# Performance work log

Hardware: AMD Instinct MI355X
Metric: run time of the kernel (lower is better)

Reference implementation:

```python
import jax, jax.numpy as jnp
import numpy as np
from jax import lax

OC = 128      # out_channels
KS = 7        # kernel_size
STRIDE = 2
IMG = 224     # image_size
NS = 7        # num_scales
PAD = KS // 2 # 3
MAXS = 2      # max_scale
EPS = 1e-5
OUT = IMG // STRIDE  # 112
B = 32
DN = ('NCHW', 'OIHW', 'NCHW')


def _windows():
    # Mirrors the torch __init__ window construction (float32 linspace like torch).
    scales = np.linspace(2.0, 1.0, NS, dtype=np.float32)
    borders = np.linspace(0, IMG // 2, NS + 1).astype(np.int64)
    iw = np.empty((NS, 4, 4), dtype=np.int64)
    for s in range(NS):
        a, b = borders[s], borders[s + 1]
        c, d = IMG - b, IMG - a
        iw[s] = np.array([[a, a, b, c], [b, a, d, b], [c, b, d, d], [a, c, c, d]])
    ow = iw // STRIDE  # output windows
    iwp = iw + PAD * MAXS
    iwp = np.stack([(iwp[s].astype(np.float32) / scales[s]).astype(np.int64) for s in range(NS)])
    iwp[:, :, :2] -= PAD
    iwp[:, :, 2:] += PAD
    return iwp, ow

IWP, OW = _windows()


def _bn(x, g, b):
    # BatchNorm2d in training mode: biased batch stats over (N, H, W)
    m = jnp.mean(x, axis=(0, 2, 3), keepdims=True)
    v = jnp.var(x, axis=(0, 2, 3), keepdims=True)
    return g[None, :, None, None] * (x - m) * lax.rsqrt(v + EPS) + b[None, :, None, None]


def _forward(inp, conv_w, gamma1, beta1, conv2_w, gamma2, beta2):
    n = inp.shape[0]
    x = jnp.pad(inp, ((0, 0), (0, 0), (PAD, PAD), (PAD, PAD)))  # ConstantPad2d(3, 0)
    out = jnp.zeros((n, OC, OUT, OUT), inp.dtype)
    for s in range(NS):
        for w in range(4):
            ti, li, bi, ri = (int(v) for v in IWP[s, w])
            crop = x[:, :, ti:bi, li:ri]
            # torch interpolate(bilinear, antialias) to the crop's own size is the identity,
            # since input_window_sizes == (bi-ti, ri-li) exactly.
            f = lax.conv_general_dilated(crop, conv_w, (STRIDE, STRIDE), 'VALID',
                                         dimension_numbers=DN)
            to, lo, bo, ro = (int(v) for v in OW[s, w])
            oh, owid = bo - to, ro - lo
            fh, fw = f.shape[2], f.shape[3]
            # torch 'nearest' (size-based): src = floor(i * in / out)
            ih = (np.arange(oh) * fh) // oh
            iwd = (np.arange(owid) * fw) // owid
            up = f[:, :, ih][:, :, :, iwd]
            out = out.at[:, :, to:bo, lo:ro].set(up)
    h = jax.nn.relu(_bn(out, gamma1, beta1))
    # MaxPool2d(kernel=3, stride=2, padding=1) -> pads with -inf
    h = lax.reduce_window(h, jnp.asarray(-jnp.inf, h.dtype), lax.max,
                          (1, 1, 3, 3), (1, 1, 2, 2),
                          ((0, 0), (0, 0), (1, 1), (1, 1)))
    h = lax.conv_general_dilated(h, conv2_w, (1, 1), ((1, 1), (1, 1)),
                                 dimension_numbers=DN)
    return jax.nn.relu(_bn(h, gamma2, beta2))


def setup_inputs() -> dict:
    key = jax.random.key(0)
    k0, k1, k2 = jax.random.split(key, 3)
    inp = jax.random.normal(k0, (B, 3, IMG, IMG), jnp.float32)
    conv_w = jax.random.normal(k1, (OC, 3, KS, KS), jnp.float32) * 0.05
    conv2_w = jax.random.normal(k2, (OC, OC, 3, 3), jnp.float32) * 0.03
    return {
        'inp': inp,
        'conv_w': conv_w,
        'gamma1': jnp.ones((OC,), jnp.float32),
        'beta1': jnp.zeros((OC,), jnp.float32),
        'conv2_w': conv2_w,
        'gamma2': jnp.ones((OC,), jnp.float32),
        'beta2': jnp.zeros((OC,), jnp.float32),
    }


def reference(inp, conv_w, gamma1, beta1, conv2_w, gamma2, beta2):
    return _forward(inp, conv_w, gamma1, beta1, conv2_w, gamma2, beta2)
```

## Files before the change

### kernel.cpp

```cpp
#include <hip/hip_runtime.h>
#include <hip/hip_bf16.h>
#include <cstdint>

#define IMGSZ 224
#define OUTSZ 112
#define POOLSZ 56
#define OCN 128
#define BN_ 32
#define PIX1 (OUTSZ*OUTSZ)
#define PIX2 (POOLSZ*POOLSZ)
#define HP 58
#define HSTRIDE (HP*HP*OCN)
#define PW 240
#define PH 233
#define PPL (PH*PW)
#define K1C 192

typedef float f32x4 __attribute__((ext_vector_type(4)));
typedef short bf16x8 __attribute__((ext_vector_type(8)));
struct alignas(4) u4a { unsigned x, y, z, w; };

__device__ inline short f2bf(float v) {
    __hip_bfloat16 h = __float2bfloat16(v);
    return *(short*)&h;
}
__device__ inline unsigned pack2bf(float a, float b) {
    return (unsigned short)f2bf(a) | ((unsigned)(unsigned short)f2bf(b) << 16);
}
__device__ inline float bf2f(short s) {
    return __uint_as_float(((unsigned)(unsigned short)s) << 16);
}
__device__ inline bf16x8 ldb8(const short* p) {
    u4a t = *(const u4a*)p;
    union { u4a u; bf16x8 v; } c; c.u = t; return c.v;
}
__device__ inline void gload16(const short* g, short* l) {
    __builtin_amdgcn_global_load_lds((const __attribute__((address_space(1))) void*)g,
                                     (__attribute__((address_space(3))) void*)l, 16, 0, 0);
}

__global__ __launch_bounds__(256) void k_setup(const float* __restrict__ w1,
                                               short* __restrict__ w1b,
                                               const float* __restrict__ w2,
                                               short* __restrict__ w2b,
                                               int2* __restrict__ map,
                                               float* __restrict__ stats,
                                               unsigned* __restrict__ h2p) {
    int blk = blockIdx.x;
    int tid = threadIdx.x;
    if (blk < 49) {
        int p = blk * 256 + tid;
        int oy = p / OUTSZ, ox = p % OUTSZ;
        int e = min(min(oy, ox), min(111 - oy, 111 - ox));
        int s = e >> 3;
        int a = 16 * s, b = a + 16, c = 224 - b, d = 224 - a;
        int ao = a >> 1, bo = b >> 1, co = c >> 1, dd = d >> 1;
        int ti, li, bi, ri;
        if      (oy >= ao && oy < bo && ox >= ao && ox < co) { ti=a; li=a; bi=b; ri=c; }
        else if (oy >= bo && oy < dd && ox >= ao && ox < bo) { ti=b; li=a; bi=d; ri=b; }
        else if (oy >= co && oy < dd && ox >= bo && ox < dd) { ti=c; li=b; bi=d; ri=d; }
        else                                                 { ti=a; li=c; bi=c; ri=d; }
        float scale = (float)(2.0 - (double)s * 0.16666666666666666);
        int tip = (int)((float)(ti + 6) / scale) - 3;
        int lip = (int)((float)(li + 6) / scale) - 3;
        int bip = (int)((float)(bi + 6) / scale) + 3;
        int rip = (int)((float)(ri + 6) / scale) + 3;
        int fh = (bip - tip - 7) / 2 + 1;
        int fw = (rip - lip - 7) / 2 + 1;
        int to = ti >> 1, lo = li >> 1, bo2 = bi >> 1, ro = ri >> 1;
        int i = oy - to, j = ox - lo;
        int pp = (i * fh) / (bo2 - to);
        int qq = (j * fw) / (ro - lo);
        map[p] = make_int2(tip + 2 * pp, lip + 2 * qq);
    } else if (blk < 145) {
        int idx = (blk - 49) * 256 + tid;
        int oc = idx / K1C, k = idx % K1C;
        int g8 = k >> 3, e2 = k & 7;
        float v = 0.f;
        if (g8 < 21 && e2 < 7) {
            int ic = g8 / 7, ky = g8 - ic * 7;
            v = w1[((oc * 3 + ic) * 7 + ky) * 7 + e2];
        }
        w1b[idx] = f2bf(v);
    } else if (blk < 721) {
        int idx = (blk - 145) * 256 + tid;
        int oc = idx / 1152;
        int rem = idx - oc * 1152;
        int ic = rem / 9;
        int s  = rem - ic * 9;
        int t  = s * 2 + (ic >> 6);
        int ic6 = ic & 63;
        int slot = (ic6 >> 3) ^ (oc & 7);
        w2b[t * 8192 + oc * 64 + slot * 8 + (ic6 & 7)] = f2bf(w2[idx]);
    } else if (blk < 785) {
        stats[(blk - 721) * 256 + tid] = 0.f;
    } else {
        int idx = blk - 785;
        int bx = idx % 57, n = idx / 57;
        int c2 = tid & 63, po = tid >> 6;
        int pp = bx * 4 + po;
        int y, x;
        if      (pp < 58)  { y = 0;  x = pp; }
        else if (pp < 116) { y = 57; x = pp - 58; }
        else if (pp < 172) { y = pp - 116 + 1; x = 0; }
        else               { y = pp - 172 + 1; x = 57; }
        h2p[(size_t)n * (HSTRIDE / 2) + (y * HP + x) * 64 + c2] = 0u;
    }
}

__global__ __launch_bounds__(256) void k_pad(const float* __restrict__ inp,
                                             short* __restrict__ padA,
                                             short* __restrict__ padB) {
    int x = threadIdx.x;
    if (x >= PW) return;
    int y = blockIdx.x;
    int pl = blockIdx.y;
    int iy = y - 3;
    bool yok = (unsigned)iy < 224u;
    const float* src = inp + (size_t)pl * 50176 + iy * 224;
    float vA = (yok && (unsigned)(x - 3) < 224u) ? src[x - 3] : 0.f;
    float vB = (yok && (unsigned)(x - 2) < 224u) ? src[x - 2] : 0.f;
    size_t o = (size_t)pl * PPL + y * PW + x;
    padA[o] = f2bf(vA);
    padB[o] = f2bf(vB);
}

__global__ __launch_bounds__(256, 4) void k_conv1m(const short* __restrict__ padA,
                                                   const short* __restrict__ padB,
                                                   const short* __restrict__ w1b,
                                                   const int2* __restrict__ map,
                                                   short* __restrict__ out1b,
                                                   float* __restrict__ sum1x,
                                                   float* __restrict__ sq1x) {
    __shared__ short As[64 * 256];
    __shared__ float sred[4][64][2];
    int tid = threadIdx.x;
    int wave = tid >> 6, lane = tid & 63;
    int q = lane >> 4, l16 = lane & 15;
    int ochalf = blockIdx.x & 1;
    int pxblk = blockIdx.x >> 1;
    int n = blockIdx.y;
    int px0 = pxblk * 128 + wave * 32 + l16;
    int px1 = px0 + 16;
    int2 m0 = map[px0];
    int2 m1 = map[px1];
    size_t bn = (size_t)n * 3 * PPL;
    const short* r0 = ((m0.y & 1) ? padB + (m0.y - 1) : padA + m0.y) + bn + m0.x * PW;
    const short* r1 = ((m1.y & 1) ? padB + (m1.y - 1) : padA + m1.y) + bn + m1.x * PW;

    const short* wsl = w1b + ochalf * 64 * K1C;
#pragma unroll
    for (int i = 0; i < 6; i++) {
        int chunk = tid + i * 256;
        int r = chunk / 24, c = chunk - r * 24;
        u4a v = *(const u4a*)(wsl + r * K1C + c * 8);
        *(u4a*)(As + r * 256 + ((c ^ (r & 15)) * 8)) = v;
    }

    bf16x8 ld[12];
#pragma unroll
    for (int icc = 0; icc < 6; icc++) {
        int g8 = (icc == 5) ? 20 : (icc * 4 + q);
        int ic = (g8 >= 7) + (g8 >= 14);
        int ky = g8 - ic * 7;
        int off = ic * PPL + ky * PW;
        ld[icc * 2]     = ldb8(r0 + off);
        ld[icc * 2 + 1] = ldb8(r1 + off);
    }

    f32x4 acc[4][2];
#pragma unroll
    for (int t = 0; t < 4; t++) { acc[t][0] = (f32x4){0,0,0,0}; acc[t][1] = (f32x4){0,0,0,0}; }

    __syncthreads();

    const short* Abase = As + l16 * 256;
#pragma unroll
    for (int icc = 0; icc < 6; icc++) {
        bf16x8 bf0 = ld[icc * 2];
        bf16x8 bf1 = ld[icc * 2 + 1];
        int pos = ((icc * 4 + q) ^ l16) * 8;
#pragma unroll
        for (int t = 0; t < 4; t++) {
            bf16x8 af = *(const bf16x8*)(Abase + t * 16 * 256 + pos);
            acc[t][0] = __builtin_amdgcn_mfma_f32_16x16x32_bf16(af, bf0, acc[t][0], 0, 0, 0);
            acc[t][1] = __builtin_amdgcn_mfma_f32_16x16x32_bf16(af, bf1, acc[t][1], 0, 0, 0);
        }
    }

    short* ob = out1b + ((size_t)(n * PIX1) + px0) * OCN + ochalf * 64 + q * 4;
#pragma unroll
    for (int t = 0; t < 4; t++) {
#pragma unroll
        for (int g = 0; g < 2; g++) {
            f32x4 a = acc[t][g];
            uint2 u;
            u.x = pack2bf(a[0], a[1]);
            u.y = pack2bf(a[2], a[3]);
            *(uint2*)(ob + (size_t)g * 16 * OCN + t * 16) = u;
        }
    }

#pragma unroll
    for (int t = 0; t < 4; t++) {
#pragma unroll
        for (int r = 0; r < 4; r++) {
            float a0 = acc[t][0][r], a1 = acc[t][1][r];
            float s = a0 + a1;
            float z = fmaf(a0, a0, a1 * a1);
#pragma unroll
            for (int msk = 1; msk < 16; msk <<= 1) {
                s += __shfl_xor(s, msk, 64);
                z += __shfl_xor(z, msk, 64);
            }
            if (l16 == 0) {
                int ocl = t * 16 + q * 4 + r;
                sred[wave][ocl][0] = s;
                sred[wave][ocl][1] = z;
            }
        }
    }
    __syncthreads();
    if (tid < 64) {
        float s = sred[0][tid][0] + sred[1][tid][0] + sred[2][tid][0] + sred[3][tid][0];
        float z = sred[0][tid][1] + sred[1][tid][1] + sred[2][tid][1] + sred[3][tid][1];
        int oc = ochalf * 64 + tid;
        atomicAdd(&sum1x[n * OCN + oc], s);
        atomicAdd(&sq1x[n * OCN + oc], z);
    }
}

__global__ void k_fin2(const float* __restrict__ sumx, const float* __restrict__ sqx,
                       const float* __restrict__ gamma, const float* __restrict__ beta,
                       float invN, float* __restrict__ scale, float* __restrict__ shift) {
    int c = threadIdx.x;
    if (c >= OCN) return;
    float s = 0.f, q = 0.f;
    for (int n = 0; n < BN_; n++) { s += sumx[n * OCN + c]; q += sqx[n * OCN + c]; }
    float m = s * invN;
    float v = q * invN - m * m;
    float sc = gamma[c] * rsqrtf(v + 1e-5f);
    scale[c] = sc;
    shift[c] = beta[c] - m * sc;
}

__global__ __launch_bounds__(256) void k_bnpool(const unsigned* __restrict__ out1b,
                                                const float* __restrict__ scale,
                                                const float* __restrict__ shift,
                                                unsigned* __restrict__ h2p) {
    int tid = threadIdx.x;
    int c2 = tid & 63, po = tid >> 6;
    int pp = blockIdx.x * 4 + po;
    int n = blockIdx.y;
    int py = pp / POOLSZ, px = pp % POOLSZ;
    const unsigned* base = out1b + (size_t)n * PIX1 * 64;
    float sc0 = scale[2 * c2],     sh0 = shift[2 * c2];
    float sc1 = scale[2 * c2 + 1], sh1 = shift[2 * c2 + 1];
    float m0 = -1e30f, m1 = -1e30f;
#pragma unroll
    for (int dy = 0; dy < 3; dy++) {
        int y = 2 * py - 1 + dy;
        if ((unsigned)y >= (unsigned)OUTSZ) continue;
#pragma unroll
        for (int dx = 0; dx < 3; dx++) {
            int x = 2 * px - 1 + dx;
            if ((unsigned)x >= (unsigned)OUTSZ) continue;
            unsigned u = base[(size_t)(y * OUTSZ + x) * 64 + c2];
            float v0 = __uint_as_float(u << 16);
            float v1 = __uint_as_float(u & 0xffff0000u);
            m0 = fmaxf(m0, fmaf(sc0, v0, sh0));
            m1 = fmaxf(m1, fmaf(sc1, v1, sh1));
        }
    }
    m0 = fmaxf(m0, 0.f); m1 = fmaxf(m1, 0.f);
    h2p[(size_t)n * (HSTRIDE / 2) + ((py + 1) * HP + (px + 1)) * 64 + c2] = pack2bf(m0, m1);
}

__global__ __launch_bounds__(256, 4) void k_conv2g(const short* __restrict__ h2p,
                                                   const short* __restrict__ w2b,
                                                   short* __restrict__ out2b,
                                                   float* __restrict__ sum2x,
                                                   float* __restrict__ sq2x) {
    __shared__ short LDSb[15360];
    int tid = threadIdx.x;
    int wave = tid >> 6, lane = tid & 63;
    int q = lane >> 4, l16 = lane & 15;
    int id = blockIdx.x;
    int xcd = id & 7, seq = id >> 3;
    int n = xcd + 8 * (seq / 28);
    int rb = seq % 28;
    int y0 = rb * 2;
    const short* hb = h2p + (size_t)n * HSTRIDE;

    int bofs[4];
#pragma unroll
    for (int i = 0; i < 4; i++) {
        int ck = tid + i * 256;
        if (ck > 895) ck = 895;
        int px = ck >> 3, sl = ck & 7;
        int r = px >= 56;
        int xc = px - (r ? 56 : 0);
        bofs[i] = ((y0 + r) * 58 + xc) * 128 + ((sl ^ (px & 7)) * 8);
    }

    f32x4 acc[2][7];
#pragma unroll
    for (int t16 = 0; t16 < 2; t16++)
#pragma unroll
        for (int g = 0; g < 7; g++) acc[t16][g] = (f32x4){0, 0, 0, 0};

    const short* Az = LDSb;
    const short* Bz = LDSb + 8192;
    int arow0 = (wave * 32 + l16) * 64;
    int arow1 = arow0 + 16 * 64;

    for (int t = 0; t < 18; t++) {
        __syncthreads();
        const short* wt = w2b + t * 8192;
#pragma unroll
        for (int i = 0; i < 4; i++)
            gload16(wt + (tid + i * 256) * 8, &LDSb[(tid + i * 256) * 8]);
        int s = t >> 1, ich = t & 1;
        int dy = s / 3, dx = s - dy * 3;
        int doff = (dy * 58 + dx) * 128 + ich * 64;
#pragma unroll
        for (int i = 0; i < 3; i++)
            gload16(hb + bofs[i] + doff, &LDSb[8192 + (tid + i * 256) * 8]);
        if (tid < 128)
            gload16(hb + bofs[3] + doff, &LDSb[8192 + (tid + 768) * 8]);
        asm volatile("s_waitcnt vmcnt(0)" ::: "memory");
        __syncthreads();
#pragma unroll
        for (int icc2 = 0; icc2 < 2; icc2++) {
            int so = ((icc2 * 4 + q) ^ (l16 & 7)) * 8;
            bf16x8 af0 = *(const bf16x8*)(Az + arow0 + so);
            bf16x8 af1 = *(const bf16x8*)(Az + arow1 + so);
            bf16x8 bf[7];
#pragma unroll
            for (int g = 0; g < 7; g++)
                bf[g] = *(const bf16x8*)(Bz + (g * 16 + l16) * 64 + so);
#pragma unroll
            for (int g = 0; g < 7; g++) {
                acc[0][g] = __builtin_amdgcn_mfma_f32_16x16x32_bf16(af0, bf[g], acc[0][g], 0, 0, 0);
                acc[1][g] = __builtin_amdgcn_mfma_f32_16x16x32_bf16(af1, bf[g], acc[1][g], 0, 0, 0);
            }
        }
    }

    short* ob = out2b + ((size_t)n * PIX2 + y0 * 56) * OCN + wave * 32 + q * 4;
#pragma unroll
    for (int t16 = 0; t16 < 2; t16++) {
#pragma unroll
        for (int g = 0; g < 7; g++) {
            f32x4 a = acc[t16][g];
            uint2 u;
            u.x = pack2bf(a[0], a[1]);
            u.y = pack2bf(a[2], a[3]);
            *(uint2*)(ob + (size_t)(g * 16 + l16) * OCN + t16 * 16) = u;
        }
    }

#pragma unroll
    for (int t16 = 0; t16 < 2; t16++) {
#pragma unroll
        for (int r = 0; r < 4; r++) {
            float sv = 0.f, zv = 0.f;
#pragma unroll
            for (int g = 0; g < 7; g++) {
                float v = acc[t16][g][r];
                sv += v;
                zv = fmaf(v, v, zv);
            }
#pragma unroll
            for (int msk = 1; msk < 16; msk <<= 1) {
                sv += __shfl_xor(sv, msk, 64);
                zv += __shfl_xor(zv, msk, 64);
            }
            if (l16 == 0) {
                int oc = wave * 32 + t16 * 16 + q * 4 + r;
                atomicAdd(&sum2x[n * OCN + oc], sv);
                atomicAdd(&sq2x[n * OCN + oc], zv);
            }
        }
    }
}

__global__ __launch_bounds__(256) void k_bnrelu(const short* __restrict__ in2,
                                                float* __restrict__ y,
                                                const float* __restrict__ scale,
                                                const float* __restrict__ shift) {
    int tid = threadIdx.x;
    int w = tid >> 6, l = tid & 63;
    int pxg = blockIdx.x * 256 + w * 64 + (l & 15) * 4;
    int n = pxg / PIX2;
    int px = pxg - n * PIX2;
    const short* src = in2 + (size_t)pxg * OCN + (l >> 4) * 8;
    float* dst = y + (size_t)n * (OCN * PIX2) + px;
#pragma unroll
    for (int jc = 0; jc < 4; jc++) {
        int c0 = (l >> 4) * 8 + jc * 32;
        bf16x8 v0 = ldb8(src + jc * 32);
        bf16x8 v1 = ldb8(src + OCN + jc * 32);
        bf16x8 v2 = ldb8(src + 2 * OCN + jc * 32);
        bf16x8 v3 = ldb8(src + 3 * OCN + jc * 32);
#pragma unroll
        for (int j = 0; j < 8; j++) {
            float sc = scale[c0 + j], sh = shift[c0 + j];
            float4 o;
            o.x = fmaxf(fmaf(sc, bf2f(v0[j]), sh), 0.f);
            o.y = fmaxf(fmaf(sc, bf2f(v1[j]), sh), 0.f);
            o.z = fmaxf(fmaf(sc, bf2f(v2[j]), sh), 0.f);
            o.w = fmaxf(fmaf(sc, bf2f(v3[j]), sh), 0.f);
            *(float4*)(dst + (size_t)(c0 + j) * PIX2) = o;
        }
    }
}

extern "C" void kernel_launch(void* const* d_in, const int* in_sizes, int n_in,
                              void* d_out, int out_size, void* d_ws, size_t ws_size,
                              hipStream_t stream) {
    const float* inp = (const float*)d_in[0];
    const float* w1  = (const float*)d_in[1];
    const float* g1  = (const float*)d_in[2];
    const float* b1  = (const float*)d_in[3];
    const float* w2  = (const float*)d_in[4];
    const float* g2  = (const float*)d_in[5];
    const float* b2  = (const float*)d_in[6];
    float* out = (float*)d_out;

    char* ws = (char*)d_ws;
    int2*  map   = (int2*)ws;
    float* stats = (float*)(ws + 102400);
    short* w2b   = (short*)(ws + 176128);
    short* w1b   = (short*)(ws + 471040);
    short* padA  = (short*)(ws + 520192);
    short* padB  = (short*)(ws + 11256832ULL);
    short* h2p   = (short*)(ws + 21993472ULL);
    short* out1b = (short*)(ws + 49551360ULL);
    short* out2b = (short*)(ws + 152311808ULL);

    float* sum1x = stats;
    float* sq1x  = stats + 4096;
    float* sum2x = stats + 8192;
    float* sq2x  = stats + 12288;
    float* SC1 = stats + 16384, *SH1 = stats + 16512;
    float* SC2 = stats + 16640, *SH2 = stats + 16768;

    k_setup <<<dim3(2609), 256, 0, stream>>>(w1, w1b, w2, w2b, map, stats, (unsigned*)h2p);
    k_pad   <<<dim3(PH, 96), 256, 0, stream>>>(inp, padA, padB);
    k_conv1m<<<dim3(196, BN_), 256, 0, stream>>>(padA, padB, w1b, map, out1b, sum1x, sq1x);
    k_fin2  <<<1, 128, 0, stream>>>(sum1x, sq1x, g1, b1, 1.f / (BN_ * PIX1), SC1, SH1);
    k_bnpool<<<dim3(PIX2 / 4, BN_), 256, 0, stream>>>((const unsigned*)out1b, SC1, SH1, (unsigned*)h2p);
    k_conv2g<<<dim3(896), 256, 0, stream>>>(h2p, w2b, out2b, sum2x, sq2x);
    k_fin2  <<<1, 128, 0, stream>>>(sum2x, sq2x, g2, b2, 1.f / (BN_ * PIX2), SC2, SH2);
    k_bnrelu<<<dim3(392), 256, 0, stream>>>(out2b, out, SC2, SH2);
}
```

Baseline: 257.5 us.

## Shrink conv tiles and LDS, use DPP row reductions, raise occupancy

Conv1 weight staging switches from a 256-stride XOR swizzle to a compact 192-stride rotated layout, cutting LDS use, and its weight load now issues after the activation loads. Conv2 retiles from two image rows (112 pixels) to 64-pixel linear blocks, with fewer accumulators, a smaller LDS buffer and 1568 blocks instead of 896. Both kernels raise the launch-bounds occupancy hint from 4 to 6 and replace shuffle-xor reductions with DPP row sums. The aim is more resident waves and cheaper reductions to hide latency, at the cost of less weight reuse per block in conv2 and more atomics.

```diff
diff --git a/kernel.cpp b/kernel.cpp
--- a/kernel.cpp
+++ b/kernel.cpp
@@ -37,6 +37,18 @@
 __device__ inline void gload16(const short* g, short* l) {
     __builtin_amdgcn_global_load_lds((const __attribute__((address_space(1))) void*)g,
                                      (__attribute__((address_space(3))) void*)l, 16, 0, 0);
+}
+
+template<int CTRL>
+__device__ inline float dppf(float v) {
+    return __int_as_float(__builtin_amdgcn_update_dpp(0, __float_as_int(v), CTRL, 0xF, 0xF, true));
+}
+__device__ inline float rowsum16(float v) {
+    v += dppf<0xB1>(v);
+    v += dppf<0x4E>(v);
+    v += dppf<0x141>(v);
+    v += dppf<0x140>(v);
+    return v;
 }
 
 __global__ __launch_bounds__(256) void k_setup(const float* __restrict__ w1,
@@ -125,15 +137,15 @@
     padB[o] = f2bf(vB);
 }
 
-__global__ __launch_bounds__(256, 4) void k_conv1m(const short* __restrict__ padA,
+__global__ __launch_bounds__(256, 6) void k_conv1m(const short* __restrict__ padA,
                                                    const short* __restrict__ padB,
                                                    const short* __restrict__ w1b,
                                                    const int2* __restrict__ map,
                                                    short* __restrict__ out1b,
                                                    float* __restrict__ sum1x,
                                                    float* __restrict__ sq1x) {
-    __shared__ short As[64 * 256];
-    __shared__ float sred[4][64][2];
+    __shared__ short As[64 * 192];
+    __shared__ float2 sred[4][64];
     int tid = threadIdx.x;
     int wave = tid >> 6, lane = tid & 63;
     int q = lane >> 4, l16 = lane & 15;
@@ -148,15 +160,6 @@
     const short* r0 = ((m0.y & 1) ? padB + (m0.y - 1) : padA + m0.y) + bn + m0.x * PW;
     const short* r1 = ((m1.y & 1) ? padB + (m1.y - 1) : padA + m1.y) + bn + m1.x * PW;
 
-    const short* wsl = w1b + ochalf * 64 * K1C;
-#pragma unroll
-    for (int i = 0; i < 6; i++) {
-        int chunk = tid + i * 256;
-        int r = chunk / 24, c = chunk - r * 24;
-        u4a v = *(const u4a*)(wsl + r * K1C + c * 8);
-        *(u4a*)(As + r * 256 + ((c ^ (r & 15)) * 8)) = v;
-    }
-
     bf16x8 ld[12];
 #pragma unroll
     for (int icc = 0; icc < 6; icc++) {
@@ -168,21 +171,40 @@
         ld[icc * 2 + 1] = ldb8(r1 + off);
     }
 
+    const short* wsl = w1b + ochalf * 64 * K1C;
+#pragma unroll
+    for (int i = 0; i < 6; i++) {
+        int chunk = tid + i * 256;
+        int r = chunk / 24, c = chunk - r * 24;
+        int rm = r % 24;
+        int sl = c + rm; if (sl >= 24) sl -= 24;
+        u4a v = *(const u4a*)(wsl + r * K1C + c * 8);
+        *(u4a*)(As + r * 192 + sl * 8) = v;
+    }
+
     f32x4 acc[4][2];
 #pragma unroll
     for (int t = 0; t < 4; t++) { acc[t][0] = (f32x4){0,0,0,0}; acc[t][1] = (f32x4){0,0,0,0}; }
 
+    int rowb[4], rowm[4];
+#pragma unroll
+    for (int t = 0; t < 4; t++) {
+        int row = t * 16 + l16;
+        rowb[t] = row * 192;
+        rowm[t] = row % 24;
+    }
+
     __syncthreads();
 
-    const short* Abase = As + l16 * 256;
 #pragma unroll
     for (int icc = 0; icc < 6; icc++) {
         bf16x8 bf0 = ld[icc * 2];
         bf16x8 bf1 = ld[icc * 2 + 1];
-        int pos = ((icc * 4 + q) ^ l16) * 8;
+        int c = icc * 4 + q;
 #pragma unroll
         for (int t = 0; t < 4; t++) {
-            bf16x8 af = *(const bf16x8*)(Abase + t * 16 * 256 + pos);
+            int sl = rowm[t] + c; if (sl >= 24) sl -= 24;
+            bf16x8 af = *(const bf16x8*)(As + rowb[t] + sl * 8);
             acc[t][0] = __builtin_amdgcn_mfma_f32_16x16x32_bf16(af, bf0, acc[t][0], 0, 0, 0);
             acc[t][1] = __builtin_amdgcn_mfma_f32_16x16x32_bf16(af, bf1, acc[t][1], 0, 0, 0);
         }
@@ -206,24 +228,17 @@
 #pragma unroll
         for (int r = 0; r < 4; r++) {
             float a0 = acc[t][0][r], a1 = acc[t][1][r];
-            float s = a0 + a1;
-            float z = fmaf(a0, a0, a1 * a1);
-#pragma unroll
-            for (int msk = 1; msk < 16; msk <<= 1) {
-                s += __shfl_xor(s, msk, 64);
-                z += __shfl_xor(z, msk, 64);
-            }
-            if (l16 == 0) {
-                int ocl = t * 16 + q * 4 + r;
-                sred[wave][ocl][0] = s;
-                sred[wave][ocl][1] = z;
-            }
+            float s = rowsum16(a0 + a1);
+            float z = rowsum16(fmaf(a0, a0, a1 * a1));
+            if (l16 == 0)
+                sred[wave][t * 16 + q * 4 + r] = make_float2(s, z);
         }
     }
     __syncthreads();
     if (tid < 64) {
-        float s = sred[0][tid][0] + sred[1][tid][0] + sred[2][tid][0] + sred[3][tid][0];
-        float z = sred[0][tid][1] + sred[1][tid][1] + sred[2][tid][1] + sred[3][tid][1];
+        float2 p0 = sred[0][tid], p1 = sred[1][tid], p2 = sred[2][tid], p3 = sred[3][tid];
+        float s = p0.x + p1.x + p2.x + p3.x;
+        float z = p0.y + p1.y + p2.y + p3.y;
         int oc = ochalf * 64 + tid;
         atomicAdd(&sum1x[n * OCN + oc], s);
         atomicAdd(&sq1x[n * OCN + oc], z);
@@ -276,38 +291,36 @@
     h2p[(size_t)n * (HSTRIDE / 2) + ((py + 1) * HP + (px + 1)) * 64 + c2] = pack2bf(m0, m1);
 }
 
-__global__ __launch_bounds__(256, 4) void k_conv2g(const short* __restrict__ h2p,
+__global__ __launch_bounds__(256, 6) void k_conv2g(const short* __restrict__ h2p,
                                                    const short* __restrict__ w2b,
                                                    short* __restrict__ out2b,
                                                    float* __restrict__ sum2x,
                                                    float* __restrict__ sq2x) {
-    __shared__ short LDSb[15360];
+    __shared__ short LDSb[12288];
     int tid = threadIdx.x;
     int wave = tid >> 6, lane = tid & 63;
     int q = lane >> 4, l16 = lane & 15;
     int id = blockIdx.x;
     int xcd = id & 7, seq = id >> 3;
-    int n = xcd + 8 * (seq / 28);
-    int rb = seq % 28;
-    int y0 = rb * 2;
+    int n = xcd + 8 * (seq / 49);
+    int px0 = (seq % 49) * 64;
     const short* hb = h2p + (size_t)n * HSTRIDE;
 
-    int bofs[4];
-#pragma unroll
-    for (int i = 0; i < 4; i++) {
+    int bofs[2];
+#pragma unroll
+    for (int i = 0; i < 2; i++) {
         int ck = tid + i * 256;
-        if (ck > 895) ck = 895;
         int px = ck >> 3, sl = ck & 7;
-        int r = px >= 56;
-        int xc = px - (r ? 56 : 0);
-        bofs[i] = ((y0 + r) * 58 + xc) * 128 + ((sl ^ (px & 7)) * 8);
-    }
-
-    f32x4 acc[2][7];
+        int p = px0 + px;
+        int y = p / POOLSZ, x = p - y * POOLSZ;
+        bofs[i] = (y * HP + x) * 128 + ((sl ^ (px & 7)) * 8);
+    }
+
+    f32x4 acc[2][4];
 #pragma unroll
     for (int t16 = 0; t16 < 2; t16++)
 #pragma unroll
-        for (int g = 0; g < 7; g++) acc[t16][g] = (f32x4){0, 0, 0, 0};
+        for (int g = 0; g < 4; g++) acc[t16][g] = (f32x4){0, 0, 0, 0};
 
     const short* Az = LDSb;
     const short* Bz = LDSb + 8192;
@@ -322,12 +335,10 @@
             gload16(wt + (tid + i * 256) * 8, &LDSb[(tid + i * 256) * 8]);
         int s = t >> 1, ich = t & 1;
         int dy = s / 3, dx = s - dy * 3;
-        int doff = (dy * 58 + dx) * 128 + ich * 64;
-#pragma unroll
-        for (int i = 0; i < 3; i++)
+        int doff = (dy * HP + dx) * 128 + ich * 64;
+#pragma unroll
+        for (int i = 0; i < 2; i++)
             gload16(hb + bofs[i] + doff, &LDSb[8192 + (tid + i * 256) * 8]);
-        if (tid < 128)
-            gload16(hb + bofs[3] + doff, &LDSb[8192 + (tid + 768) * 8]);
         asm volatile("s_waitcnt vmcnt(0)" ::: "memory");
         __syncthreads();
 #pragma unroll
@@ -335,23 +346,23 @@
             int so = ((icc2 * 4 + q) ^ (l16 & 7)) * 8;
             bf16x8 af0 = *(const bf16x8*)(Az + arow0 + so);
             bf16x8 af1 = *(const bf16x8*)(Az + arow1 + so);
-            bf16x8 bf[7];
-#pragma unroll
-            for (int g = 0; g < 7; g++)
+            bf16x8 bf[4];
+#pragma unroll
+            for (int g = 0; g < 4; g++)
                 bf[g] = *(const bf16x8*)(Bz + (g * 16 + l16) * 64 + so);
 #pragma unroll
-            for (int g = 0; g < 7; g++) {
+            for (int g = 0; g < 4; g++) {
                 acc[0][g] = __builtin_amdgcn_mfma_f32_16x16x32_bf16(af0, bf[g], acc[0][g], 0, 0, 0);
                 acc[1][g] = __builtin_amdgcn_mfma_f32_16x16x32_bf16(af1, bf[g], acc[1][g], 0, 0, 0);
             }
         }
     }
 
-    short* ob = out2b + ((size_t)n * PIX2 + y0 * 56) * OCN + wave * 32 + q * 4;
+    short* ob = out2b + ((size_t)n * PIX2 + px0) * OCN + wave * 32 + q * 4;
 #pragma unroll
     for (int t16 = 0; t16 < 2; t16++) {
 #pragma unroll
-        for (int g = 0; g < 7; g++) {
+        for (int g = 0; g < 4; g++) {
             f32x4 a = acc[t16][g];
             uint2 u;
             u.x = pack2bf(a[0], a[1]);
@@ -366,16 +377,13 @@
         for (int r = 0; r < 4; r++) {
             float sv = 0.f, zv = 0.f;
 #pragma unroll
-            for (int g = 0; g < 7; g++) {
+            for (int g = 0; g < 4; g++) {
                 float v = acc[t16][g][r];
                 sv += v;
                 zv = fmaf(v, v, zv);
             }
-#pragma unroll
-            for (int msk = 1; msk < 16; msk <<= 1) {
-                sv += __shfl_xor(sv, msk, 64);
-                zv += __shfl_xor(zv, msk, 64);
-            }
+            sv = rowsum16(sv);
+            zv = rowsum16(zv);
             if (l16 == 0) {
                 int oc = wave * 32 + t16 * 16 + q * 4 + r;
                 atomicAdd(&sum2x[n * OCN + oc], sv);
@@ -451,7 +459,7 @@
     k_conv1m<<<dim3(196, BN_), 256, 0, stream>>>(padA, padB, w1b, map, out1b, sum1x, sq1x);
     k_fin2  <<<1, 128, 0, stream>>>(sum1x, sq1x, g1, b1, 1.f / (BN_ * PIX1), SC1, SH1);
     k_bnpool<<<dim3(PIX2 / 4, BN_), 256, 0, stream>>>((const unsigned*)out1b, SC1, SH1, (unsigned*)h2p);
-    k_conv2g<<<dim3(896), 256, 0, stream>>>(h2p, w2b, out2b, sum2x, sq2x);
+    k_conv2g<<<dim3(1568), 256, 0, stream>>>(h2p, w2b, out2b, sum2x, sq2x);
     k_fin2  <<<1, 128, 0, stream>>>(sum2x, sq2x, g2, b2, 1.f / (BN_ * PIX2), SC2, SH2);
     k_bnrelu<<<dim3(392), 256, 0, stream>>>(out2b, out, SC2, SH2);
 }
```

After: 299.8 us. +16.4%, slower.
